# Optimization experiments

Hardware: AMD Instinct MI355X
Metric: run time of the kernel (lower is better)

## Reference

```python
import jax, jax.numpy as jnp
import numpy as np
from jax import lax

B, NP = 4, 8192          # events, points per event (equal-sized batches)
RATIO, R, K = 0.25, 0.2, 64
MP = int(NP * RATIO)     # sampled centers per event
D_IN = 32
BIG = 1e10


def _fps_one(pos):
    # Farthest point sampling (deterministic start at index 0). pos: [NP,3] -> [MP] int32
    d = jnp.sum((pos - pos[0]) ** 2, axis=-1)
    sel = jnp.zeros((MP,), jnp.int32)

    def body(i, carry):
        sel, d = carry
        nxt = jnp.argmax(d).astype(jnp.int32)
        sel = sel.at[i].set(nxt)
        d = jnp.minimum(d, jnp.sum((pos - pos[nxt]) ** 2, axis=-1))
        return sel, d

    sel, _ = lax.fori_loop(1, MP, body, (sel, d))
    return sel


def _ball_query_one(centers, pos):
    # centers: [MP,3], pos: [NP,3] -> neighbor idx [MP,K] int32, validity mask [MP,K]
    d2 = jnp.sum((centers[:, None, :] - pos[None, :, :]) ** 2, axis=-1)  # [MP,NP]
    d2m = jnp.where(d2 <= R * R, d2, BIG)
    neg, idx = lax.top_k(-d2m, K)          # K nearest within radius (deterministic)
    mask = (-neg) <= R * R
    return idx.astype(jnp.int32), mask


def reference(x, pos, batch, W1, b1, W2, b2, W3, b3):
    xb = x.reshape(B, NP, D_IN)
    pb = pos.reshape(B, NP, 3)

    sel = jax.vmap(_fps_one)(pb)                                   # [B,MP]
    centers = jnp.take_along_axis(pb, sel[..., None], axis=1)      # [B,MP,3]
    idx, mask = jax.vmap(_ball_query_one)(centers, pb)             # [B,MP,K]

    gather = jax.vmap(lambda a, i: a[i])
    pos_j = gather(pb, idx)                                        # [B,MP,K,3]
    x_j = gather(xb, idx)                                          # [B,MP,K,D_IN]

    rel = pos_j - centers[:, :, None, :]
    h = jnp.concatenate([x_j, rel], axis=-1)                       # [B,MP,K,D_IN+3]
    h = jax.nn.relu(h @ W1 + b1)
    h = jax.nn.relu(h @ W2 + b2)
    h = jax.nn.relu(h @ W3 + b3)                                   # [B,MP,K,128]

    h = jnp.where(mask[..., None], h, -BIG)
    x_out = jnp.max(h, axis=2).reshape(B * MP, -1)                 # max aggregation
    pos_out = centers.reshape(B * MP, 3)
    batch_out = jnp.repeat(jnp.arange(B, dtype=jnp.int32), MP)
    return x_out, pos_out, batch_out


def setup_inputs() -> dict:
    key = jax.random.key(0)
    ks = jax.random.split(key, 8)
    x = jax.random.normal(ks[0], (B * NP, D_IN), jnp.float32)
    pos = jax.random.uniform(ks[1], (B * NP, 3), jnp.float32)
    batch = (jnp.arange(B * NP) // NP).astype(jnp.int64)
    W1 = jax.random.normal(ks[2], (D_IN + 3, 64), jnp.float32) * 0.05
    b1 = jnp.zeros((64,), jnp.float32)
    W2 = jax.random.normal(ks[3], (64, 64), jnp.float32) * 0.05
    b2 = jnp.zeros((64,), jnp.float32)
    W3 = jax.random.normal(ks[4], (64, 128), jnp.float32) * 0.05
    b3 = jnp.zeros((128,), jnp.float32)
    return {"x": x, "pos": pos, "batch": batch, "W1": W1, "b1": b1,
            "W2": W2, "b2": b2, "W3": W3, "b3": b3}
```

## Files before the change

kernel.cpp:

```cpp
#include <hip/hip_runtime.h>


#define BATCH 4
#define NP 8192
#define MP 2048
#define KNN 64
#define DIN 32

#define DPP_FMAX(v, ctrl)                                                     \
  {                                                                           \
    int _t = __builtin_amdgcn_update_dpp(__float_as_int(v),                   \
                                         __float_as_int(v), (ctrl), 0xF,      \
                                         0xF, false);                         \
    (v) = fmaxf((v), __int_as_float(_t));                                     \
  }

__global__ __launch_bounds__(1024) void fps_k(const float* __restrict__ pos,
                                              float* __restrict__ pout,
                                              float* __restrict__ bout)
{
  const int b = blockIdx.x;
  const int tid = threadIdx.x;
  const int lane = tid & 63, wid = tid >> 6;
  const float* __restrict__ pb = pos + (size_t)b * NP * 3;
  const int base = tid * 8;

  bout[b * MP + tid] = (float)b;
  bout[b * MP + 1024 + tid] = (float)b;

  float px[8], py[8], pz[8], d[8];
#pragma unroll
  for (int k = 0; k < 8; k++) {
    px[k] = pb[(base + k) * 3 + 0];
    py[k] = pb[(base + k) * 3 + 1];
    pz[k] = pb[(base + k) * 3 + 2];
  }
  const float c0x = pb[0], c0y = pb[1], c0z = pb[2];
  if (tid == 0) {
    pout[(size_t)b * MP * 3 + 0] = c0x;
    pout[(size_t)b * MP * 3 + 1] = c0y;
    pout[(size_t)b * MP * 3 + 2] = c0z;
  }

  float bv = -1.f;
#pragma unroll
  for (int k = 0; k < 8; k++) {
    float dx = px[k] - c0x, dy = py[k] - c0y, dz = pz[k] - c0z;
    float nd = dx * dx + dy * dy + dz * dz;
    d[k] = nd;
    bv = fmaxf(bv, nd);
  }

  __shared__ float sv[2][16];
  __shared__ __align__(16) float sc[2][16][4];

  for (int i = 1; i < MP; i++) {
    float v = bv;
    DPP_FMAX(v, 0x111);
    DPP_FMAX(v, 0x112);
    DPP_FMAX(v, 0x114);
    DPP_FMAX(v, 0x118);
    DPP_FMAX(v, 0x142);
    DPP_FMAX(v, 0x143);
    const float wmax =
        __int_as_float(__builtin_amdgcn_readlane(__float_as_int(v), 63));

    unsigned long long m = __ballot(bv == wmax);
    const int src = (int)__builtin_ctzll(m);
    const int p = i & 1;
    if (lane == src) {
      float ox = px[7], oy = py[7], oz = pz[7];
#pragma unroll
      for (int k = 6; k >= 0; k--)
        if (d[k] == wmax) { ox = px[k]; oy = py[k]; oz = pz[k]; }
      sv[p][wid] = wmax;
      float4 q; q.x = ox; q.y = oy; q.z = oz; q.w = 0.f;
      *(float4*)&sc[p][wid][0] = q;
    }
    __syncthreads();

    float v2 = sv[p][lane & 15];
    float v2r = v2;
    DPP_FMAX(v2r, 0x111);
    DPP_FMAX(v2r, 0x112);
    DPP_FMAX(v2r, 0x114);
    DPP_FMAX(v2r, 0x118);
    const float mv =
        __int_as_float(__builtin_amdgcn_readlane(__float_as_int(v2r), 15));
    unsigned long long m2 = __ballot(v2 == mv);
    const int mw = (int)__builtin_ctzll(m2);
    const float4 cc = *(const float4*)&sc[p][mw][0];
    const float ncx = cc.x, ncy = cc.y, ncz = cc.z;

    if (tid == 0) {
      pout[((size_t)b * MP + i) * 3 + 0] = ncx;
      pout[((size_t)b * MP + i) * 3 + 1] = ncy;
      pout[((size_t)b * MP + i) * 3 + 2] = ncz;
    }

    bv = -1.f;
#pragma unroll
    for (int k = 0; k < 8; k++) {
      float dx = px[k] - ncx, dy = py[k] - ncy, dz = pz[k] - ncz;
      float nd = dx * dx + dy * dy + dz * dz;
      float dn = fminf(d[k], nd);
      d[k] = dn;
      bv = fmaxf(bv, dn);
    }
  }
}

__global__ __launch_bounds__(64) void ballq_k(const float* __restrict__ pos,
                                              const float* __restrict__ pout,
                                              int* __restrict__ nbr)
{
  const int wg = blockIdx.x;
  const int lane = threadIdx.x;
  const int b = wg >> 11;
  const float* __restrict__ pb = pos + (size_t)b * NP * 3;
  const float cx = pout[(size_t)wg * 3 + 0];
  const float cy = pout[(size_t)wg * 3 + 1];
  const float cz = pout[(size_t)wg * 3 + 2];
  const float R2 = (float)(0.2 * 0.2);

  __shared__ unsigned long long cand[1024];
  int cnt = 0;
  for (int basej = 0; basej < NP; basej += 64) {
    const int j = basej + lane;
    float dx = pb[j * 3 + 0] - cx;
    float dy = pb[j * 3 + 1] - cy;
    float dz = pb[j * 3 + 2] - cz;
    float d2 = dx * dx + dy * dy + dz * dz;
    bool in = (d2 <= R2);
    unsigned long long mb = __ballot(in);
    int pre = (int)__popcll(mb & ((1ull << lane) - 1ull));
    int slot = cnt + pre;
    if (in && slot < 1024)
      cand[slot] = ((unsigned long long)__float_as_uint(d2) << 32) | (unsigned int)j;
    cnt += (int)__popcll(mb);
  }
  if (cnt > 1024) cnt = 1024;

  int myout = -1;
  for (int r = 0; r < KNN; r++) {
    unsigned long long v = ~0ull; int slot = -1;
    for (int s = lane; s < cnt; s += 64) {
      unsigned long long c = cand[s];
      if (c < v) { v = c; slot = s; }
    }
#pragma unroll
    for (int off = 1; off < 64; off <<= 1) {
      unsigned long long ov = __shfl_xor(v, off);
      int os = __shfl_xor(slot, off);
      if (ov < v) { v = ov; slot = os; }
    }
    if (lane == r) myout = (v == ~0ull) ? -1 : (int)(v & 0xffffffffu);
    if (lane == 0 && slot >= 0) cand[slot] = ~0ull;
    __syncthreads();
  }
  nbr[(size_t)wg * KNN + lane] = myout;
}

__global__ __launch_bounds__(64) void p1_k(const float* __restrict__ x,
                                           const float* __restrict__ W1,
                                           float* __restrict__ P1)
{
  const int j = blockIdx.x;
  const int c = threadIdx.x;
  const float* __restrict__ xr = x + (size_t)j * DIN;
  float acc = 0.f;
#pragma unroll
  for (int k = 0; k < DIN; k++) acc += xr[k] * W1[k * 64 + c];
  P1[(size_t)j * 64 + c] = acc;
}

__global__ __launch_bounds__(256) void tw_k(const float* __restrict__ W2,
                                            const float* __restrict__ W3,
                                            float* __restrict__ W2T,
                                            float* __restrict__ W3T)
{
  int e = blockIdx.x * 256 + threadIdx.x;
  if (e < 64 * 64) {
    int c = e >> 6, k = e & 63;
    W2T[e] = W2[k * 64 + c];
  } else {
    int e2 = e - 64 * 64;
    if (e2 < 128 * 64) {
      int c = e2 >> 6, k = e2 & 63;
      W3T[e2] = W3[k * 128 + c];
    }
  }
}

__global__ __launch_bounds__(64) void mlp_k(const float* __restrict__ pos,
    const float* __restrict__ P1, const float* __restrict__ W1,
    const float* __restrict__ b1, const float* __restrict__ W2T,
    const float* __restrict__ b2, const float* __restrict__ W3T,
    const float* __restrict__ b3, const int* __restrict__ nbr,
    const float* __restrict__ pout, float* __restrict__ xout)
{
  __shared__ __align__(16) float h2s[64 * 68];
  const int wg = blockIdx.x;
  const int lane = threadIdx.x;
  const int b = wg >> 11;
  const int idx = nbr[(size_t)wg * KNN + lane];
  const bool valid = idx >= 0;
  const int j = valid ? idx : 0;
  const float cx = pout[(size_t)wg * 3 + 0];
  const float cy = pout[(size_t)wg * 3 + 1];
  const float cz = pout[(size_t)wg * 3 + 2];
  const float* __restrict__ pj = pos + ((size_t)b * NP + j) * 3;
  const float rx = pj[0] - cx, ry = pj[1] - cy, rz = pj[2] - cz;
  const float* __restrict__ p1r =
      (const float*)__builtin_assume_aligned(P1 + ((size_t)b * NP + j) * 64, 16);

  float h1[64];
#pragma unroll
  for (int k = 0; k < 64; k++) {
    float v = p1r[k] + rx * W1[32 * 64 + k] + ry * W1[33 * 64 + k]
                     + rz * W1[34 * 64 + k] + b1[k];
    h1[k] = fmaxf(v, 0.f);
  }

  for (int c4 = 0; c4 < 16; c4++) {
    float a0 = b2[c4 * 4 + 0], a1 = b2[c4 * 4 + 1];
    float a2 = b2[c4 * 4 + 2], a3 = b2[c4 * 4 + 3];
    const float* __restrict__ w0 = W2T + (c4 * 4 + 0) * 64;
    const float* __restrict__ w1 = W2T + (c4 * 4 + 1) * 64;
    const float* __restrict__ w2 = W2T + (c4 * 4 + 2) * 64;
    const float* __restrict__ w3 = W2T + (c4 * 4 + 3) * 64;
#pragma unroll
    for (int k = 0; k < 64; k++) {
      a0 += h1[k] * w0[k]; a1 += h1[k] * w1[k];
      a2 += h1[k] * w2[k]; a3 += h1[k] * w3[k];
    }
    float4 q;
    q.x = fmaxf(a0, 0.f); q.y = fmaxf(a1, 0.f);
    q.z = fmaxf(a2, 0.f); q.w = fmaxf(a3, 0.f);
    *(float4*)&h2s[lane * 68 + c4 * 4] = q;
  }

  float4 keep = make_float4(0.f, 0.f, 0.f, 0.f);
  const float* __restrict__ h2p = &h2s[lane * 68];
  for (int c4 = 0; c4 < 32; c4++) {
    float a0 = b3[c4 * 4 + 0], a1 = b3[c4 * 4 + 1];
    float a2 = b3[c4 * 4 + 2], a3 = b3[c4 * 4 + 3];
    const float* __restrict__ w0 = W3T + (c4 * 4 + 0) * 64;
    const float* __restrict__ w1 = W3T + (c4 * 4 + 1) * 64;
    const float* __restrict__ w2 = W3T + (c4 * 4 + 2) * 64;
    const float* __restrict__ w3 = W3T + (c4 * 4 + 3) * 64;
#pragma unroll
    for (int k4 = 0; k4 < 16; k4++) {
      float4 h = *(const float4*)&h2p[k4 * 4];
      a0 += h.x * w0[k4 * 4 + 0]; a0 += h.y * w0[k4 * 4 + 1];
      a0 += h.z * w0[k4 * 4 + 2]; a0 += h.w * w0[k4 * 4 + 3];
      a1 += h.x * w1[k4 * 4 + 0]; a1 += h.y * w1[k4 * 4 + 1];
      a1 += h.z * w1[k4 * 4 + 2]; a1 += h.w * w1[k4 * 4 + 3];
      a2 += h.x * w2[k4 * 4 + 0]; a2 += h.y * w2[k4 * 4 + 1];
      a2 += h.z * w2[k4 * 4 + 2]; a2 += h.w * w2[k4 * 4 + 3];
      a3 += h.x * w3[k4 * 4 + 0]; a3 += h.y * w3[k4 * 4 + 1];
      a3 += h.z * w3[k4 * 4 + 2]; a3 += h.w * w3[k4 * 4 + 3];
    }
    a0 = valid ? fmaxf(a0, 0.f) : 0.f;
    a1 = valid ? fmaxf(a1, 0.f) : 0.f;
    a2 = valid ? fmaxf(a2, 0.f) : 0.f;
    a3 = valid ? fmaxf(a3, 0.f) : 0.f;
#pragma unroll
    for (int off = 1; off < 64; off <<= 1) {
      a0 = fmaxf(a0, __shfl_xor(a0, off));
      a1 = fmaxf(a1, __shfl_xor(a1, off));
      a2 = fmaxf(a2, __shfl_xor(a2, off));
      a3 = fmaxf(a3, __shfl_xor(a3, off));
    }
    if (lane == c4) { keep.x = a0; keep.y = a1; keep.z = a2; keep.w = a3; }
  }
  if (lane < 32)
    *(float4*)&xout[(size_t)wg * 128 + lane * 4] = keep;
}

extern "C" void kernel_launch(void* const* d_in, const int* in_sizes, int n_in,
                              void* d_out, int out_size, void* d_ws, size_t ws_size,
                              hipStream_t stream)
{
  const float* x   = (const float*)d_in[0];
  const float* pos = (const float*)d_in[1];
  const float* W1 = (const float*)d_in[3];
  const float* b1 = (const float*)d_in[4];
  const float* W2 = (const float*)d_in[5];
  const float* b2 = (const float*)d_in[6];
  const float* W3 = (const float*)d_in[7];
  const float* b3 = (const float*)d_in[8];

  float* out  = (float*)d_out;
  float* xout = out;
  float* pout = out + 8192 * 128;
  float* bout = out + 8192 * 128 + 8192 * 3;

  char* ws = (char*)d_ws;
  float* P1  = (float*)ws;
  float* W2T = (float*)(ws + 8388608);
  float* W3T = (float*)(ws + 8404992);
  int*   nbr = (int*)(ws + 8437760);

  fps_k<<<dim3(BATCH), dim3(1024), 0, stream>>>(pos, pout, bout);
  p1_k<<<dim3(BATCH * NP), dim3(64), 0, stream>>>(x, W1, P1);
  tw_k<<<dim3(48), dim3(256), 0, stream>>>(W2, W3, W2T, W3T);
  ballq_k<<<dim3(BATCH * MP), dim3(64), 0, stream>>>(pos, pout, nbr);
  mlp_k<<<dim3(BATCH * MP), dim3(64), 0, stream>>>(pos, P1, W1, b1, W2T, b2,
                                                   W3T, b3, nbr, pout, xout);
}
```

Measured before the change: 2.808 ms.

## Halve FPS workgroup to 512 threads using packed FP32 math and index-based winner lookup

The farthest point sampling kernel now runs 512 threads per batch, each holding 16 points as packed float2 pairs. Distance updates use v_pk_add/mul/fma_f32. Each wave publishes a single 64-bit value-plus-index to shared memory, and the winning center's coordinates are reloaded from global memory (likely an L1/L2 hit) instead of being passed through LDS. This shrinks the per-iteration barrier and cross-wave reduction to 8 waves and cuts the VALU instruction count. In exchange each thread runs a longer serial loop and the critical path gains a dependent global load on every iteration.

```diff
diff --git a/kernel.cpp b/kernel.cpp
--- a/kernel.cpp
+++ b/kernel.cpp
@@ -15,26 +15,49 @@
     (v) = fmaxf((v), __int_as_float(_t));                                     \
   }
 
-__global__ __launch_bounds__(1024) void fps_k(const float* __restrict__ pos,
-                                              float* __restrict__ pout,
-                                              float* __restrict__ bout)
+typedef float v2f __attribute__((ext_vector_type(2)));
+
+__device__ __forceinline__ v2f pk_add(v2f a, v2f b) {
+  v2f r;
+  asm("v_pk_add_f32 %0, %1, %2" : "=v"(r) : "v"(a), "v"(b));
+  return r;
+}
+__device__ __forceinline__ v2f pk_mul(v2f a, v2f b) {
+  v2f r;
+  asm("v_pk_mul_f32 %0, %1, %2" : "=v"(r) : "v"(a), "v"(b));
+  return r;
+}
+__device__ __forceinline__ v2f pk_fma(v2f a, v2f b, v2f c) {
+  v2f r;
+  asm("v_pk_fma_f32 %0, %1, %2, %3" : "=v"(r) : "v"(a), "v"(b), "v"(c));
+  return r;
+}
+
+__global__ __launch_bounds__(512) void fps_k(const float* __restrict__ pos,
+                                             float* __restrict__ pout,
+                                             float* __restrict__ bout)
 {
   const int b = blockIdx.x;
   const int tid = threadIdx.x;
   const int lane = tid & 63, wid = tid >> 6;
   const float* __restrict__ pb = pos + (size_t)b * NP * 3;
-  const int base = tid * 8;
-
-  bout[b * MP + tid] = (float)b;
-  bout[b * MP + 1024 + tid] = (float)b;
-
-  float px[8], py[8], pz[8], d[8];
-#pragma unroll
-  for (int k = 0; k < 8; k++) {
-    px[k] = pb[(base + k) * 3 + 0];
-    py[k] = pb[(base + k) * 3 + 1];
-    pz[k] = pb[(base + k) * 3 + 2];
-  }
+  const int base = tid * 16;
+
+#pragma unroll
+  for (int q = 0; q < 4; q++) bout[b * MP + q * 512 + tid] = (float)b;
+
+  float t[48];
+  const float4* __restrict__ pv = (const float4*)(pb + (size_t)base * 3);
+#pragma unroll
+  for (int q = 0; q < 12; q++) *(float4*)&t[q * 4] = pv[q];
+
+  v2f px[8], py[8], pz[8], d[8];
+#pragma unroll
+  for (int j = 0; j < 8; j++) {
+    px[j].x = t[6 * j + 0]; py[j].x = t[6 * j + 1]; pz[j].x = t[6 * j + 2];
+    px[j].y = t[6 * j + 3]; py[j].y = t[6 * j + 4]; pz[j].y = t[6 * j + 5];
+  }
+
   const float c0x = pb[0], c0y = pb[1], c0z = pb[2];
   if (tid == 0) {
     pout[(size_t)b * MP * 3 + 0] = c0x;
@@ -42,17 +65,20 @@
     pout[(size_t)b * MP * 3 + 2] = c0z;
   }
 
+  v2f cxn = {-c0x, -c0x}, cyn = {-c0y, -c0y}, czn = {-c0z, -c0z};
   float bv = -1.f;
 #pragma unroll
-  for (int k = 0; k < 8; k++) {
-    float dx = px[k] - c0x, dy = py[k] - c0y, dz = pz[k] - c0z;
-    float nd = dx * dx + dy * dy + dz * dz;
-    d[k] = nd;
-    bv = fmaxf(bv, nd);
-  }
-
-  __shared__ float sv[2][16];
-  __shared__ __align__(16) float sc[2][16][4];
+  for (int j = 0; j < 8; j++) {
+    v2f dx = pk_add(px[j], cxn);
+    v2f dy = pk_add(py[j], cyn);
+    v2f dz = pk_add(pz[j], czn);
+    v2f nd = pk_fma(dx, dx, pk_mul(dy, dy));
+    nd = pk_fma(dz, dz, nd);
+    d[j] = nd;
+    bv = fmaxf(bv, fmaxf(nd.x, nd.y));
+  }
+
+  __shared__ unsigned long long slt[2][8];
 
   for (int i = 1; i < MP; i++) {
     float v = bv;
@@ -65,32 +91,35 @@
     const float wmax =
         __int_as_float(__builtin_amdgcn_readlane(__float_as_int(v), 63));
 
-    unsigned long long m = __ballot(bv == wmax);
+    const unsigned long long m = __ballot(bv == wmax);
     const int src = (int)__builtin_ctzll(m);
     const int p = i & 1;
     if (lane == src) {
-      float ox = px[7], oy = py[7], oz = pz[7];
-#pragma unroll
-      for (int k = 6; k >= 0; k--)
-        if (d[k] == wmax) { ox = px[k]; oy = py[k]; oz = pz[k]; }
-      sv[p][wid] = wmax;
-      float4 q; q.x = ox; q.y = oy; q.z = oz; q.w = 0.f;
-      *(float4*)&sc[p][wid][0] = q;
+      int ks = 15;
+#pragma unroll
+      for (int k = 14; k >= 0; k--) {
+        float dv = (k & 1) ? d[k >> 1].y : d[k >> 1].x;
+        if (dv == wmax) ks = k;
+      }
+      slt[p][wid] = ((unsigned long long)__float_as_uint(wmax) << 32)
+                    | (unsigned)(base + ks);
     }
     __syncthreads();
 
-    float v2 = sv[p][lane & 15];
+    const unsigned long long kv = slt[p][lane & 7];
+    const float v2 = __uint_as_float((unsigned)(kv >> 32));
     float v2r = v2;
     DPP_FMAX(v2r, 0x111);
     DPP_FMAX(v2r, 0x112);
     DPP_FMAX(v2r, 0x114);
-    DPP_FMAX(v2r, 0x118);
     const float mv =
-        __int_as_float(__builtin_amdgcn_readlane(__float_as_int(v2r), 15));
-    unsigned long long m2 = __ballot(v2 == mv);
+        __int_as_float(__builtin_amdgcn_readlane(__float_as_int(v2r), 7));
+    const unsigned long long m2 = __ballot(v2 == mv);
     const int mw = (int)__builtin_ctzll(m2);
-    const float4 cc = *(const float4*)&sc[p][mw][0];
-    const float ncx = cc.x, ncy = cc.y, ncz = cc.z;
+    const int js = __builtin_amdgcn_readlane((int)(unsigned)kv, mw);
+    const float ncx = pb[js * 3 + 0];
+    const float ncy = pb[js * 3 + 1];
+    const float ncz = pb[js * 3 + 2];
 
     if (tid == 0) {
       pout[((size_t)b * MP + i) * 3 + 0] = ncx;
@@ -98,14 +127,22 @@
       pout[((size_t)b * MP + i) * 3 + 2] = ncz;
     }
 
+    cxn = (v2f){-ncx, -ncx};
+    cyn = (v2f){-ncy, -ncy};
+    czn = (v2f){-ncz, -ncz};
     bv = -1.f;
 #pragma unroll
-    for (int k = 0; k < 8; k++) {
-      float dx = px[k] - ncx, dy = py[k] - ncy, dz = pz[k] - ncz;
-      float nd = dx * dx + dy * dy + dz * dz;
-      float dn = fminf(d[k], nd);
-      d[k] = dn;
-      bv = fmaxf(bv, dn);
+    for (int j = 0; j < 8; j++) {
+      v2f dx = pk_add(px[j], cxn);
+      v2f dy = pk_add(py[j], cyn);
+      v2f dz = pk_add(pz[j], czn);
+      v2f nd = pk_fma(dx, dx, pk_mul(dy, dy));
+      nd = pk_fma(dz, dz, nd);
+      v2f dn;
+      dn.x = fminf(d[j].x, nd.x);
+      dn.y = fminf(d[j].y, nd.y);
+      d[j] = dn;
+      bv = fmaxf(bv, fmaxf(dn.x, dn.y));
     }
   }
 }
@@ -302,7 +339,7 @@
   float* W3T = (float*)(ws + 8404992);
   int*   nbr = (int*)(ws + 8437760);
 
-  fps_k<<<dim3(BATCH), dim3(1024), 0, stream>>>(pos, pout, bout);
+  fps_k<<<dim3(BATCH), dim3(512), 0, stream>>>(pos, pout, bout);
   p1_k<<<dim3(BATCH * NP), dim3(64), 0, stream>>>(x, W1, P1);
   tw_k<<<dim3(48), dim3(256), 0, stream>>>(W2, W3, W2T, W3T);
   ballq_k<<<dim3(BATCH * MP), dim3(64), 0, stream>>>(pos, pout, nbr);
```

Result: slower. 2.889 ms (+2.9%).

## Vectorize FPS distance updates with packed float2 and stage points in LDS

Applied to the files above, without the earlier changes.

The FPS kernel now loads each thread's 8 points with float4 vector loads and copies the whole point cloud into shared memory. It holds coordinates and distances as float2 vectors so the compiler can emit packed FP32 math. The per-iteration winner exchange writes a packed (max value, point index) 64-bit word instead of the float value plus a float4 of coordinates. The new center's coordinates are read back from the shared table by index. This cuts per-iteration ALU work and the shared-memory traffic on the serial 2047-step critical path, but adds a 96KB shared-memory allocation and a dependent LDS read after the index is chosen.

```diff
diff --git a/kernel.cpp b/kernel.cpp
--- a/kernel.cpp
+++ b/kernel.cpp
@@ -15,6 +15,8 @@
     (v) = fmaxf((v), __int_as_float(_t));                                     \
   }
 
+typedef float v2f __attribute__((ext_vector_type(2)));
+
 __global__ __launch_bounds__(1024) void fps_k(const float* __restrict__ pos,
                                               float* __restrict__ pout,
                                               float* __restrict__ bout)
@@ -28,13 +30,23 @@
   bout[b * MP + tid] = (float)b;
   bout[b * MP + 1024 + tid] = (float)b;
 
-  float px[8], py[8], pz[8], d[8];
-#pragma unroll
-  for (int k = 0; k < 8; k++) {
-    px[k] = pb[(base + k) * 3 + 0];
-    py[k] = pb[(base + k) * 3 + 1];
-    pz[k] = pb[(base + k) * 3 + 2];
-  }
+  __shared__ __align__(16) float ptab[NP * 3];
+  __shared__ unsigned long long slt[2][16];
+
+  float t[24];
+  const float4* __restrict__ pv = (const float4*)(pb + (size_t)tid * 24);
+#pragma unroll
+  for (int q = 0; q < 6; q++) *(float4*)&t[q * 4] = pv[q];
+#pragma unroll
+  for (int q = 0; q < 6; q++) *(float4*)&ptab[tid * 24 + q * 4] = *(float4*)&t[q * 4];
+
+  v2f px[4], py[4], pz[4], d[4];
+#pragma unroll
+  for (int j = 0; j < 4; j++) {
+    px[j].x = t[6 * j + 0]; py[j].x = t[6 * j + 1]; pz[j].x = t[6 * j + 2];
+    px[j].y = t[6 * j + 3]; py[j].y = t[6 * j + 4]; pz[j].y = t[6 * j + 5];
+  }
+
   const float c0x = pb[0], c0y = pb[1], c0z = pb[2];
   if (tid == 0) {
     pout[(size_t)b * MP * 3 + 0] = c0x;
@@ -43,16 +55,16 @@
   }
 
   float bv = -1.f;
-#pragma unroll
-  for (int k = 0; k < 8; k++) {
-    float dx = px[k] - c0x, dy = py[k] - c0y, dz = pz[k] - c0z;
-    float nd = dx * dx + dy * dy + dz * dz;
-    d[k] = nd;
-    bv = fmaxf(bv, nd);
-  }
-
-  __shared__ float sv[2][16];
-  __shared__ __align__(16) float sc[2][16][4];
+  {
+    v2f cx = {c0x, c0x}, cy = {c0y, c0y}, cz = {c0z, c0z};
+#pragma unroll
+    for (int j = 0; j < 4; j++) {
+      v2f dx = px[j] - cx, dy = py[j] - cy, dz = pz[j] - cz;
+      v2f nd = dx * dx + dy * dy + dz * dz;
+      d[j] = nd;
+      bv = fmaxf(bv, fmaxf(nd.x, nd.y));
+    }
+  }
 
   for (int i = 1; i < MP; i++) {
     float v = bv;
@@ -65,21 +77,23 @@
     const float wmax =
         __int_as_float(__builtin_amdgcn_readlane(__float_as_int(v), 63));
 
-    unsigned long long m = __ballot(bv == wmax);
+    const unsigned long long m = __ballot(bv == wmax);
     const int src = (int)__builtin_ctzll(m);
     const int p = i & 1;
     if (lane == src) {
-      float ox = px[7], oy = py[7], oz = pz[7];
-#pragma unroll
-      for (int k = 6; k >= 0; k--)
-        if (d[k] == wmax) { ox = px[k]; oy = py[k]; oz = pz[k]; }
-      sv[p][wid] = wmax;
-      float4 q; q.x = ox; q.y = oy; q.z = oz; q.w = 0.f;
-      *(float4*)&sc[p][wid][0] = q;
+      int ks = 7;
+#pragma unroll
+      for (int k = 6; k >= 0; k--) {
+        float dv = (k & 1) ? d[k >> 1].y : d[k >> 1].x;
+        if (dv == wmax) ks = k;
+      }
+      slt[p][wid] = ((unsigned long long)__float_as_uint(wmax) << 32)
+                    | (unsigned)(base + ks);
     }
     __syncthreads();
 
-    float v2 = sv[p][lane & 15];
+    const unsigned long long kv = slt[p][lane & 15];
+    const float v2 = __uint_as_float((unsigned)(kv >> 32));
     float v2r = v2;
     DPP_FMAX(v2r, 0x111);
     DPP_FMAX(v2r, 0x112);
@@ -87,10 +101,12 @@
     DPP_FMAX(v2r, 0x118);
     const float mv =
         __int_as_float(__builtin_amdgcn_readlane(__float_as_int(v2r), 15));
-    unsigned long long m2 = __ballot(v2 == mv);
+    const unsigned long long m2 = __ballot(v2 == mv);
     const int mw = (int)__builtin_ctzll(m2);
-    const float4 cc = *(const float4*)&sc[p][mw][0];
-    const float ncx = cc.x, ncy = cc.y, ncz = cc.z;
+    const int js = __builtin_amdgcn_readlane((int)(unsigned)kv, mw);
+    const float ncx = ptab[js * 3 + 0];
+    const float ncy = ptab[js * 3 + 1];
+    const float ncz = ptab[js * 3 + 2];
 
     if (tid == 0) {
       pout[((size_t)b * MP + i) * 3 + 0] = ncx;
@@ -98,14 +114,17 @@
       pout[((size_t)b * MP + i) * 3 + 2] = ncz;
     }
 
+    const v2f cx = {ncx, ncx}, cy = {ncy, ncy}, cz = {ncz, ncz};
     bv = -1.f;
 #pragma unroll
-    for (int k = 0; k < 8; k++) {
-      float dx = px[k] - ncx, dy = py[k] - ncy, dz = pz[k] - ncz;
-      float nd = dx * dx + dy * dy + dz * dz;
-      float dn = fminf(d[k], nd);
-      d[k] = dn;
-      bv = fmaxf(bv, dn);
+    for (int j = 0; j < 4; j++) {
+      v2f dx = px[j] - cx, dy = py[j] - cy, dz = pz[j] - cz;
+      v2f nd = dx * dx + dy * dy + dz * dz;
+      v2f dn;
+      dn.x = fminf(d[j].x, nd.x);
+      dn.y = fminf(d[j].y, nd.y);
+      d[j] = dn;
+      bv = fmaxf(bv, fmaxf(dn.x, dn.y));
     }
   }
 }
```

Measured after the change: 2.554 ms. -9.0%, faster.
